# Optimization experiments

Hardware: AMD Instinct MI355X
Metric: run time of the kernel (lower is better)

The kernel has to match this reference:

```python
import jax, jax.numpy as jnp
import numpy as np
import math

DIM, NH, HD = 4096, 32, 128
B, S = 2, 2048
MAX_SEQ, INIT_SLICE = 4096, 2048  # init_slice = max_seq_len - max_prompt_size
NEG = -1e9


def setup_inputs() -> dict:
    key = jax.random.key(0)
    ks = jax.random.split(key, 6)
    x = jax.random.normal(ks[0], (B, S, DIM), dtype=jnp.float32)
    scale = 1.0 / math.sqrt(DIM)
    wq = jax.random.normal(ks[1], (DIM, DIM), dtype=jnp.float32) * scale
    wk = jax.random.normal(ks[2], (DIM, DIM), dtype=jnp.float32) * scale
    wv = jax.random.normal(ks[3], (DIM, DIM), dtype=jnp.float32) * scale
    wo = jax.random.normal(ks[4], (DIM, DIM), dtype=jnp.float32) * scale
    # RoPE frequencies, viewed as real pairs [S, HD//2, 2] = (cos, sin)
    inv_freq = 1.0 / (10000.0 ** (jnp.arange(0, HD, 2, dtype=jnp.float32) / HD))
    ang = jnp.arange(S, dtype=jnp.float32)[:, None] * inv_freq[None, :]  # [S, HD//2]
    freqs_cis_real = jnp.stack([jnp.cos(ang), jnp.sin(ang)], axis=-1)
    # causal additive mask [1,1,S,S]
    mask = jnp.where(jnp.triu(jnp.ones((S, S), dtype=bool), k=1), NEG, 0.0)[None, None].astype(jnp.float32)
    cache_k = jnp.zeros((B, MAX_SEQ, NH, HD), dtype=jnp.float32)
    cache_v = jnp.zeros((B, MAX_SEQ, NH, HD), dtype=jnp.float32)
    return {"x": x, "freqs_cis_real": freqs_cis_real, "mask": mask,
            "wq": wq, "wk": wk, "wv": wv, "wo": wo,
            "cache_k": cache_k, "cache_v": cache_v, "slice_size": 2048}


def _apply_rotary(xq, xk, freqs_cis_real):
    # xq, xk: [b, s, h, d]; pairs along last dim are (real, imag)
    b, s, h, d = xq.shape
    fr = freqs_cis_real[None, :, None, :, 0]  # [1, s, 1, d//2]
    fi = freqs_cis_real[None, :, None, :, 1]

    def rot(t):
        t = t.reshape(b, s, h, d // 2, 2)
        tr, ti = t[..., 0], t[..., 1]
        out = jnp.stack([tr * fr - ti * fi, tr * fi + ti * fr], axis=-1)
        return out.reshape(b, s, h, d)

    return rot(xq), rot(xk)


def reference(x, freqs_cis_real, mask, wq, wk, wv, wo, cache_k, cache_v, slice_size):
    bsz, seqlen, _ = x.shape
    xq = (x @ wq.T).reshape(bsz, seqlen, NH, HD)
    xk = (x @ wk.T).reshape(bsz, seqlen, NH, HD)
    xv = (x @ wv.T).reshape(bsz, seqlen, NH, HD)
    xq, xk = _apply_rotary(xq, xk, freqs_cis_real)
    # prompt-phase (seqlen > 1) cache update: cat(cache[:, :init_slice], new)
    cache_k_new = jnp.concatenate([cache_k[:bsz, :INIT_SLICE], xk], axis=1)
    cache_v_new = jnp.concatenate([cache_v[:bsz, :INIT_SLICE], xv], axis=1)
    keys = cache_k_new[:, -slice_size:]    # [b, k, h, d]
    values = cache_v_new[:, -slice_size:]
    scores = jnp.einsum('bqhd,bkhd->bhqk', xq, keys) / math.sqrt(HD)
    scores = scores + mask
    probs = jax.nn.softmax(scores.astype(jnp.float32), axis=-1).astype(xq.dtype)
    out = jnp.einsum('bhqk,bkhd->bqhd', probs, values).reshape(bsz, seqlen, -1)
    return out @ wo.T
```

## Files before the change

### kernel.cpp

```cpp
#include <hip/hip_runtime.h>
#include <hip/hip_bf16.h>
#include <stdint.h>

#define SEQ   2048
#define NHEAD 32
#define HDIM  128
#define DMODEL 4096
#define MTOT  4096
#define RSCALE 0.08838834764831845f

typedef __hip_bfloat16 bf16_t;
typedef __attribute__((ext_vector_type(8))) short short8v;
typedef __attribute__((ext_vector_type(4))) short short4v;
typedef __attribute__((ext_vector_type(4))) float f32x4;

typedef __attribute__((address_space(3))) void lds_void;
typedef __attribute__((address_space(1))) void gbl_void;
#define TO_LDS(p) ((lds_void*)(uint32_t)(uintptr_t)(p))
#define TO_GBL(p) ((gbl_void*)(uintptr_t)(p))
#define ASYNC_CP16(g, l) __builtin_amdgcn_global_load_lds(TO_GBL(g), TO_LDS(l), 16, 0, 0)

__device__ __forceinline__ float bf2f(short u) {
  union { uint32_t i; float f; } x; x.i = ((uint32_t)(uint16_t)u) << 16; return x.f;
}

__global__ __launch_bounds__(256) void cast4_f32_to_bf16(const float* __restrict__ s0,
                                                         const float* __restrict__ s1,
                                                         const float* __restrict__ s2,
                                                         const float* __restrict__ s3,
                                                         bf16_t* __restrict__ out) {
  const int w = blockIdx.y;
  const float* in = (w == 0) ? s0 : ((w == 1) ? s1 : ((w == 2) ? s2 : s3));
  bf16_t* o = out + (size_t)w * 16777216u;
  size_t i = (size_t)blockIdx.x * 256 + threadIdx.x;
  const f32x4* p = (const f32x4*)in + i * 2;
  f32x4 a = p[0], b = p[1];
  __align__(16) bf16_t tmp[8];
#pragma unroll
  for (int j = 0; j < 4; ++j) tmp[j]     = __float2bfloat16(a[j]);
#pragma unroll
  for (int j = 0; j < 4; ++j) tmp[4 + j] = __float2bfloat16(b[j]);
  *(short8v*)(o + i * 8) = *(const short8v*)tmp;
}

__global__ __launch_bounds__(256) void cast_f32_to_bf16(const float* __restrict__ in,
                                                        bf16_t* __restrict__ out) {
  size_t i = (size_t)blockIdx.x * 256 + threadIdx.x;
  const f32x4* p = (const f32x4*)in + i * 2;
  f32x4 a = p[0], b = p[1];
  __align__(16) bf16_t tmp[8];
#pragma unroll
  for (int j = 0; j < 4; ++j) tmp[j]     = __float2bfloat16(a[j]);
#pragma unroll
  for (int j = 0; j < 4; ++j) tmp[4 + j] = __float2bfloat16(b[j]);
  *(short8v*)(out + i * 8) = *(const short8v*)tmp;
}

#define VMW_(N) asm volatile("s_waitcnt vmcnt(" #N ")" ::: "memory")
#define VMW(N) VMW_(N)
#define SB0 __builtin_amdgcn_sched_barrier(0)

#define STAGE_A(mh_, X)                                                        \
  { const int tr_ = tid >> 3, c_ = tid & 7;                                    \
    _Pragma("unroll")                                                          \
    for (int i_ = 0; i_ < 2; ++i_) {                                           \
      const int row_ = (mh_) * 64 + i_ * 128 + tr_;                            \
      const int cg_ = c_ ^ (row_ & 7);                                         \
      ASYNC_CP16(gA0 + (size_t)row_ * 4096 + (size_t)(X) * 64 + cg_ * 8,       \
                 ldsc + (((X) & 1) << 16) + row_ * 128 + c_ * 16); } }

#define STAGE_B(nh_, X)                                                        \
  { const int tr_ = tid >> 3, c_ = tid & 7;                                    \
    _Pragma("unroll")                                                          \
    for (int i_ = 0; i_ < 2; ++i_) {                                           \
      const int row_ = i_ * 128 + (tr_ >> 5) * 64 + (nh_) * 32 + (tr_ & 31);   \
      const int cg_ = c_ ^ (row_ & 7);                                         \
      ASYNC_CP16(gB0 + (size_t)row_ * 4096 + (size_t)(X) * 64 + cg_ * 8,       \
                 ldsc + (((X) & 1) << 16) + 32768 + row_ * 128 + c_ * 16); } }

#define TILE4(T, DOSTG, VA, VB, VC)                                            \
  {                                                                            \
    const int sb = ((T) & 1) << 16;                                            \
    const int Xn = (T) + 1;                                                    \
    short8v a0[4][2], a1[4][2], b0[2][2], b1[2][2];                            \
                                                 \
    VMW(VA);                                                                   \
    __builtin_amdgcn_s_barrier();                                              \
    SB0;                                                                       \
    if (DOSTG) STAGE_A(0, Xn);                                                 \
    SB0;                                                                       \
    _Pragma("unroll") for (int m = 0; m < 4; ++m)                              \
      _Pragma("unroll") for (int kk = 0; kk < 2; ++kk)                         \
        a0[m][kk] = *(const short8v*)(ldsc + sb + aRow + m * 2048 + (kk ? cx1 : cx0)); \
    _Pragma("unroll") for (int n = 0; n < 2; ++n)                              \
      _Pragma("unroll") for (int kk = 0; kk < 2; ++kk)                         \
        b0[n][kk] = *(const short8v*)(ldsc + sb + bRow + n * 2048 + (kk ? cx1 : cx0)); \
    __builtin_amdgcn_s_setprio(1);                                             \
    _Pragma("unroll") for (int m = 0; m < 4; ++m)                              \
      _Pragma("unroll") for (int n = 0; n < 2; ++n)                            \
        _Pragma("unroll") for (int kk = 0; kk < 2; ++kk)                       \
          acc[m][n] = __builtin_amdgcn_mfma_f32_16x16x32_bf16(a0[m][kk], b0[n][kk], acc[m][n], 0, 0, 0); \
    __builtin_amdgcn_s_setprio(0);                                             \
                                                 \
    VMW(VB);                                                                   \
    __builtin_amdgcn_s_barrier();                                              \
    SB0;                                                                       \
    if (DOSTG) STAGE_B(0, Xn);                                                 \
    SB0;                                                                       \
    _Pragma("unroll") for (int n = 0; n < 2; ++n)                              \
      _Pragma("unroll") for (int kk = 0; kk < 2; ++kk)                         \
        b1[n][kk] = *(const short8v*)(ldsc + sb + bRow + 4096 + n * 2048 + (kk ? cx1 : cx0)); \
    __builtin_amdgcn_s_setprio(1);                                             \
    _Pragma("unroll") for (int m = 0; m < 4; ++m)                              \
      _Pragma("unroll") for (int n = 0; n < 2; ++n)                            \
        _Pragma("unroll") for (int kk = 0; kk < 2; ++kk)                       \
          acc[m][2 + n] = __builtin_amdgcn_mfma_f32_16x16x32_bf16(a0[m][kk], b1[n][kk], acc[m][2 + n], 0, 0, 0); \
    __builtin_amdgcn_s_setprio(0);                                             \
                                                 \
    VMW(VC);                                                                   \
    __builtin_amdgcn_s_barrier();                                              \
    SB0;                                                                       \
    if (DOSTG) STAGE_B(1, Xn);                                                 \
    SB0;                                                                       \
    _Pragma("unroll") for (int m = 0; m < 4; ++m)                              \
      _Pragma("unroll") for (int kk = 0; kk < 2; ++kk)                         \
        a1[m][kk] = *(const short8v*)(ldsc + sb + aRow + 8192 + m * 2048 + (kk ? cx1 : cx0)); \
    __builtin_amdgcn_s_setprio(1);                                             \
    _Pragma("unroll") for (int m = 0; m < 4; ++m)                              \
      _Pragma("unroll") for (int n = 0; n < 2; ++n)                            \
        _Pragma("unroll") for (int kk = 0; kk < 2; ++kk)                       \
          acc[4 + m][2 + n] = __builtin_amdgcn_mfma_f32_16x16x32_bf16(a1[m][kk], b1[n][kk], acc[4 + m][2 + n], 0, 0, 0); \
    __builtin_amdgcn_s_setprio(0);                                             \
                                     \
    if (DOSTG) STAGE_A(1, Xn);                                                 \
    __builtin_amdgcn_s_setprio(1);                                             \
    _Pragma("unroll") for (int m = 0; m < 4; ++m)                              \
      _Pragma("unroll") for (int n = 0; n < 2; ++n)                            \
        _Pragma("unroll") for (int kk = 0; kk < 2; ++kk)                       \
          acc[4 + m][n] = __builtin_amdgcn_mfma_f32_16x16x32_bf16(a1[m][kk], b0[n][kk], acc[4 + m][n], 0, 0, 0); \
    __builtin_amdgcn_s_setprio(0);                                             \
  }

template <bool OUT_BF16>
__global__ __launch_bounds__(512, 2) void gemm_nt(const bf16_t* __restrict__ A,
                                                  const bf16_t* __restrict__ B0,
                                                  const bf16_t* __restrict__ B1,
                                                  const bf16_t* __restrict__ B2,
                                                  void* __restrict__ Cout) {
  __shared__ __align__(16) char ldsbuf[131072];
  char* ldsc = ldsbuf;
  const int z = blockIdx.z;
  const bf16_t* __restrict__ Bm = (z == 0) ? B0 : (z == 1 ? B1 : B2);
  const int tid = threadIdx.x;
  const int wave = tid >> 6, lane = tid & 63;
  const int bid = blockIdx.x;
  const int xcd = bid & 7, idx = bid >> 3;
  const int bm = (xcd >> 1) * 4 + (idx >> 3);
  const int bn = (xcd & 1) * 8 + (idx & 7);
  const int wr = wave >> 2, wc = wave & 3;
  const int r = lane & 15, g = lane >> 4;

  f32x4 acc[8][4] = {};

  const bf16_t* gA0 = A  + (size_t)bm * 256 * 4096;
  const bf16_t* gB0 = Bm + (size_t)bn * 256 * 4096;

  const int swz = r & 7;
  const int cx0 = (g ^ swz) << 4;
  const int cx1 = ((4 + g) ^ swz) << 4;
  const int aRow = (wr * 128 + r) * 128;
  const int bRow = 32768 + (wc * 64 + r) * 128;

  STAGE_A(0, 0);
  STAGE_B(0, 0);
  STAGE_B(1, 0);
  STAGE_A(1, 0);

  for (int T = 0; T < 63; ++T) TILE4(T, 1, 4, 4, 4);
  TILE4(63, 0, 4, 2, 0);

  const size_t row_base = (size_t)bm * 256 + wr * 128 + g * 4;
  const size_t col_base = (size_t)bn * 256 + wc * 64 + r;
  if (OUT_BF16) {
    bf16_t* C = (bf16_t*)Cout + (size_t)z * 16777216u;
#pragma unroll
    for (int m = 0; m < 8; ++m)
#pragma unroll
      for (int n = 0; n < 4; ++n)
#pragma unroll
        for (int j = 0; j < 4; ++j)
          C[(row_base + m * 16 + j) * 4096 + col_base + n * 16] = __float2bfloat16(acc[m][n][j]);
  } else {
    float* C = (float*)Cout;
#pragma unroll
    for (int m = 0; m < 8; ++m)
#pragma unroll
      for (int n = 0; n < 4; ++n)
#pragma unroll
        for (int j = 0; j < 4; ++j)
          C[(row_base + m * 16 + j) * 4096 + col_base + n * 16] = acc[m][n][j];
  }
}

__global__ __launch_bounds__(256) void rope_kernel(const bf16_t* __restrict__ qkv,
                                                   const float* __restrict__ freqs,
                                                   bf16_t* __restrict__ qrot,
                                                   bf16_t* __restrict__ krot) {
  const int which = blockIdx.y;
  const bf16_t* __restrict__ src = qkv + (size_t)which * 16777216u;
  bf16_t* __restrict__ dst = (which == 0) ? qrot : krot;
  const float sc = (which == 0) ? RSCALE : 1.0f;
  size_t t = (size_t)blockIdx.x * 256 + threadIdx.x;
  int dg = t & 15;
  int s  = (int)(t >> 4) & 2047;
  int bh = (int)(t >> 15);
  int b  = bh >> 5;
  int d0 = dg * 8;

  short8v v = *(const short8v*)&src[((size_t)(b * 2048 + s)) * 4096 + (bh & 31) * 128 + d0];
  const float* fp = freqs + (size_t)s * 128 + d0;
  f32x4 f0 = *(const f32x4*)fp;
  f32x4 f1 = *(const f32x4*)(fp + 4);
  float fr[4] = {f0[0], f0[2], f1[0], f1[2]};
  float fi[4] = {f0[1], f0[3], f1[1], f1[3]};
  __align__(16) bf16_t tmp[8];
#pragma unroll
  for (int i = 0; i < 4; ++i) {
    float tr = bf2f(v[2 * i]), ti = bf2f(v[2 * i + 1]);
    tmp[2 * i]     = __float2bfloat16((tr * fr[i] - ti * fi[i]) * sc);
    tmp[2 * i + 1] = __float2bfloat16((tr * fi[i] + ti * fr[i]) * sc);
  }
  *(short8v*)&dst[((size_t)bh * 2048 + s) * 128 + d0] = *(const short8v*)tmp;
}

__global__ __launch_bounds__(256) void vtrans_kernel(const bf16_t* __restrict__ xv,
                                                     bf16_t* __restrict__ vt) {
  __shared__ bf16_t tile[64 * 136];
  const int s0 = blockIdx.x * 64;
  const int bh = blockIdx.y;
  const int b = bh >> 5, h = bh & 31;
  const int tid = threadIdx.x;
#pragma unroll
  for (int it = 0; it < 4; ++it) {
    int c = it * 256 + tid;
    int row = c >> 4, col8 = c & 15;
    short8v v = *(const short8v*)&xv[((size_t)(b * 2048 + s0 + row)) * 4096 + h * 128 + col8 * 8];
    *(short8v*)&tile[row * 136 + col8 * 8] = v;
  }
  __syncthreads();
#pragma unroll
  for (int it = 0; it < 4; ++it) {
    int c = it * 256 + tid;
    int d = c >> 3, sc = c & 7;
    __align__(16) bf16_t tmp[8];
#pragma unroll
    for (int i = 0; i < 8; ++i) tmp[i] = tile[(sc * 8 + i) * 136 + d];
    *(short8v*)&vt[((size_t)(bh * 128 + d)) * 2048 + s0 + sc * 8] = *(const short8v*)tmp;
  }
}

#define PSTR 72
__global__ __launch_bounds__(512) void attn_kernel(const bf16_t* __restrict__ qrot,
                                                   const bf16_t* __restrict__ krot,
                                                   const bf16_t* __restrict__ vt,
                                                   bf16_t* __restrict__ att) {
  __shared__ bf16_t Kls[3][64 * 128];
  __shared__ bf16_t Vls[3][128 * 64];
  __shared__ bf16_t Pls[8][16 * PSTR];

  const int lid  = blockIdx.x;
  const int xcd  = lid & 7;
  const int kk_  = lid >> 3;
  const int bh   = xcd + 8 * ((kk_ >> 4) & 7);
  const int qidx = 15 - (kk_ & 15);
  const int warp = threadIdx.x >> 6;
  const int lane = threadIdx.x & 63;
  const int r = lane & 15, g = lane >> 4;

  const bf16_t* __restrict__ Q  = qrot + (size_t)bh * 2048 * 128;
  const bf16_t* __restrict__ Kp = krot + (size_t)bh * 2048 * 128;
  const bf16_t* __restrict__ Vt = vt   + (size_t)bh * 128 * 2048;
  bf16_t* __restrict__ Pw = &Pls[warp][0];

  const int qB = qidx * 128 + warp * 16;
  const int ntiles = 2 * qidx + 2;

  short8v qf[4];
#pragma unroll
  for (int kk = 0; kk < 4; ++kk)
    qf[kk] = *(const short8v*)&Q[(size_t)(qB + r) * 128 + kk * 32 + g * 8];

  float l = 0.f;
  f32x4 o[8];
#pragma unroll
  for (int n2 = 0; n2 < 8; ++n2) o[n2] = f32x4{0.f, 0.f, 0.f, 0.f};

  const int rA = lane >> 4, cA = lane & 15;
  const int rB = lane >> 3, cB = lane & 7;
  const int swz = (r & 7) << 4;

  auto STG = [&](int kb_, int buf) {
#pragma unroll
    for (int i = 0; i < 2; ++i) {
      const int krow = warp * 8 + i * 4 + rA;
      const int kcol = 8 * (cA ^ (krow & 7));
      ASYNC_CP16(Kp + (size_t)(kb_ + krow) * 128 + kcol,
                 (char*)&Kls[buf][0] + (size_t)(krow * 128 + cA * 8) * 2);
    }
#pragma unroll
    for (int i = 0; i < 2; ++i) {
      const int vrow = warp * 16 + i * 8 + rB;
      const int vcol = 8 * (cB ^ rB);
      ASYNC_CP16(Vt + (size_t)vrow * 2048 + kb_ + vcol,
                 (char*)&Vls[buf][0] + (size_t)(vrow * 64 + cB * 8) * 2);
    }
  };

  STG(0, 0);
  int cur = 0;
  for (int t = 0; t < ntiles; ++t) {
    const int kb = t * 64;
    const int nxt = (cur == 2) ? 0 : cur + 1;
    if (t + 1 < ntiles) {
      STG(kb + 64, nxt);
      VMW(4);
    } else {
      VMW(0);
    }
    __builtin_amdgcn_s_barrier();
    SB0;

    if (kb <= qB + 15) {
      const char* Kc = (const char*)&Kls[cur][0];
      const char* Vc = (const char*)&Vls[cur][0];
      f32x4 sacc[4];
#pragma unroll
      for (int n = 0; n < 4; ++n) sacc[n] = f32x4{0.f, 0.f, 0.f, 0.f};
#pragma unroll
      for (int n = 0; n < 4; ++n)
#pragma unroll
        for (int kk = 0; kk < 4; ++kk) {
          short8v kf = *(const short8v*)(Kc + (n * 16 + r) * 256 + ((kk * 64 + g * 16) ^ swz));
          sacc[n] = __builtin_amdgcn_mfma_f32_16x16x32_bf16(kf, qf[kk], sacc[n], 0, 0, 0);
        }

      float p[16];
#pragma unroll
      for (int n = 0; n < 4; ++n)
#pragma unroll
        for (int j = 0; j < 4; ++j)
          p[n * 4 + j] = __expf(sacc[n][j]);

      if (kb + 63 > qB) {
        const int qa = qB + r;
#pragma unroll
        for (int n = 0; n < 4; ++n)
#pragma unroll
          for (int j = 0; j < 4; ++j)
            if (kb + n * 16 + g * 4 + j > qa) p[n * 4 + j] = 0.f;
      }

      {
        float ts[8];
#pragma unroll
        for (int i = 0; i < 8; ++i) ts[i] = p[i] + p[i + 8];
#pragma unroll
        for (int i = 0; i < 4; ++i) ts[i] += ts[i + 4];
        float rs = (ts[0] + ts[1]) + (ts[2] + ts[3]);
        rs += __shfl_xor(rs, 16, 64);
        rs += __shfl_xor(rs, 32, 64);
        l += rs;
      }

#pragma unroll
      for (int n = 0; n < 4; ++n) {
        __align__(8) bf16_t tp[4];
#pragma unroll
        for (int j = 0; j < 4; ++j) tp[j] = __float2bfloat16(p[n * 4 + j]);
        *(short4v*)&Pw[r * PSTR + n * 16 + g * 4] = *(const short4v*)tp;
      }

#pragma unroll
      for (int kk2 = 0; kk2 < 2; ++kk2) {
        short8v pf = *(const short8v*)&Pw[r * PSTR + kk2 * 32 + g * 8];
#pragma unroll
        for (int n2 = 0; n2 < 8; ++n2) {
          short8v vf = *(const short8v*)(Vc + (n2 * 16 + r) * 128 + ((kk2 * 64 + g * 16) ^ swz));
          o[n2] = __builtin_amdgcn_mfma_f32_16x16x32_bf16(pf, vf, o[n2], 0, 0, 0);
        }
      }
    }
    cur = nxt;
  }

  float lq[4];
#pragma unroll
  for (int j = 0; j < 4; ++j) lq[j] = 1.0f / __shfl(l, g * 4 + j, 64);
  const int b = bh >> 5, h = bh & 31;
#pragma unroll
  for (int n2 = 0; n2 < 8; ++n2)
#pragma unroll
    for (int j = 0; j < 4; ++j)
      att[((size_t)(b * 2048 + qB + g * 4 + j)) * 4096 + h * 128 + n2 * 16 + r] =
          __float2bfloat16(o[n2][j] * lq[j]);
}

extern "C" void kernel_launch(void* const* d_in, const int* in_sizes, int n_in,
                              void* d_out, int out_size, void* d_ws, size_t ws_size,
                              hipStream_t stream) {
  (void)in_sizes; (void)n_in; (void)out_size; (void)ws_size;
  const float* x  = (const float*)d_in[0];
  const float* fr = (const float*)d_in[1];
  const float* wq = (const float*)d_in[3];
  const float* wk = (const float*)d_in[4];
  const float* wv = (const float*)d_in[5];
  const float* wo = (const float*)d_in[6];

  char* ws = (char*)d_ws;
  const size_t MB32 = 33554432;
  bf16_t* xb  = (bf16_t*)(ws + 0 * MB32);
  bf16_t* wqb = (bf16_t*)(ws + 1 * MB32);
  bf16_t* wkb = (bf16_t*)(ws + 2 * MB32);
  bf16_t* wvb = (bf16_t*)(ws + 3 * MB32);
  bf16_t* qkv = (bf16_t*)(ws + 4 * MB32);

  cast4_f32_to_bf16<<<dim3(8192, 4), 256, 0, stream>>>(x, wq, wk, wv, xb);

  gemm_nt<true><<<dim3(256, 1, 3), 512, 0, stream>>>(xb, wqb, wkb, wvb, (void*)qkv);

  bf16_t* qrot = xb;
  bf16_t* krot = wqb;
  bf16_t* vtp  = wkb;
  bf16_t* attb = wvb;

  rope_kernel<<<dim3(8192, 2), 256, 0, stream>>>(qkv, fr, qrot, krot);
  vtrans_kernel<<<dim3(32, 64), 256, 0, stream>>>(qkv + 2 * 16777216u, vtp);

  bf16_t* wob = qkv;
  cast_f32_to_bf16<<<8192, 256, 0, stream>>>(wo, wob);

  attn_kernel<<<1024, 512, 0, stream>>>(qrot, krot, vtp, attb);

  gemm_nt<false><<<dim3(256, 1, 1), 512, 0, stream>>>(attb, wob, wob, wob, d_out);
}
```

Measured before the change: 676.9 us.

## Fuse RoPE and V transpose into QKV GEMM epilogue, reorder LDS staging

The QKV GEMM epilogue now applies rotary embedding (with the query scale) using a lane shuffle to fetch each pair partner, and writes V directly in transposed layout. This removes the separate rope and vtrans kernels and their round trip of the QKV intermediate through global memory. Inside the GEMM tile loop, async global-to-LDS staging is moved after the LDS fragment reads and followed by an explicit lgkmcnt wait. The block-to-tile mapping across XCDs is also changed. In exchange, the epilogue does scattered 2-byte and 8-byte stores and extra freq loads per element, which may slow the GEMM tail.

```diff
diff --git a/kernel.cpp b/kernel.cpp
--- a/kernel.cpp
+++ b/kernel.cpp
@@ -87,14 +87,15 @@
     VMW(VA);                                                                   \
     __builtin_amdgcn_s_barrier();                                              \
     SB0;                                                                       \
-    if (DOSTG) STAGE_A(0, Xn);                                                 \
-    SB0;                                                                       \
     _Pragma("unroll") for (int m = 0; m < 4; ++m)                              \
       _Pragma("unroll") for (int kk = 0; kk < 2; ++kk)                         \
         a0[m][kk] = *(const short8v*)(ldsc + sb + aRow + m * 2048 + (kk ? cx1 : cx0)); \
     _Pragma("unroll") for (int n = 0; n < 2; ++n)                              \
       _Pragma("unroll") for (int kk = 0; kk < 2; ++kk)                         \
         b0[n][kk] = *(const short8v*)(ldsc + sb + bRow + n * 2048 + (kk ? cx1 : cx0)); \
+    if (DOSTG) STAGE_A(0, Xn);                                                 \
+    asm volatile("s_waitcnt lgkmcnt(0)" ::: "memory");                         \
+    SB0;                                                                       \
     __builtin_amdgcn_s_setprio(1);                                             \
     _Pragma("unroll") for (int m = 0; m < 4; ++m)                              \
       _Pragma("unroll") for (int n = 0; n < 2; ++n)                            \
@@ -105,11 +106,12 @@
     VMW(VB);                                                                   \
     __builtin_amdgcn_s_barrier();                                              \
     SB0;                                                                       \
-    if (DOSTG) STAGE_B(0, Xn);                                                 \
-    SB0;                                                                       \
     _Pragma("unroll") for (int n = 0; n < 2; ++n)                              \
       _Pragma("unroll") for (int kk = 0; kk < 2; ++kk)                         \
         b1[n][kk] = *(const short8v*)(ldsc + sb + bRow + 4096 + n * 2048 + (kk ? cx1 : cx0)); \
+    if (DOSTG) STAGE_B(0, Xn);                                                 \
+    asm volatile("s_waitcnt lgkmcnt(0)" ::: "memory");                         \
+    SB0;                                                                       \
     __builtin_amdgcn_s_setprio(1);                                             \
     _Pragma("unroll") for (int m = 0; m < 4; ++m)                              \
       _Pragma("unroll") for (int n = 0; n < 2; ++n)                            \
@@ -120,11 +122,12 @@
     VMW(VC);                                                                   \
     __builtin_amdgcn_s_barrier();                                              \
     SB0;                                                                       \
-    if (DOSTG) STAGE_B(1, Xn);                                                 \
-    SB0;                                                                       \
     _Pragma("unroll") for (int m = 0; m < 4; ++m)                              \
       _Pragma("unroll") for (int kk = 0; kk < 2; ++kk)                         \
         a1[m][kk] = *(const short8v*)(ldsc + sb + aRow + 8192 + m * 2048 + (kk ? cx1 : cx0)); \
+    if (DOSTG) STAGE_B(1, Xn);                                                 \
+    asm volatile("s_waitcnt lgkmcnt(0)" ::: "memory");                         \
+    SB0;                                                                       \
     __builtin_amdgcn_s_setprio(1);                                             \
     _Pragma("unroll") for (int m = 0; m < 4; ++m)                              \
       _Pragma("unroll") for (int n = 0; n < 2; ++n)                            \
@@ -141,12 +144,15 @@
     __builtin_amdgcn_s_setprio(0);                                             \
   }
 
-template <bool OUT_BF16>
+template <int MODE>
 __global__ __launch_bounds__(512, 2) void gemm_nt(const bf16_t* __restrict__ A,
                                                   const bf16_t* __restrict__ B0,
                                                   const bf16_t* __restrict__ B1,
                                                   const bf16_t* __restrict__ B2,
-                                                  void* __restrict__ Cout) {
+                                                  void* __restrict__ out0,
+                                                  bf16_t* __restrict__ out1,
+                                                  bf16_t* __restrict__ out2,
+                                                  const float* __restrict__ freqs) {
   __shared__ __align__(16) char ldsbuf[131072];
   char* ldsc = ldsbuf;
   const int z = blockIdx.z;
@@ -155,8 +161,8 @@
   const int wave = tid >> 6, lane = tid & 63;
   const int bid = blockIdx.x;
   const int xcd = bid & 7, idx = bid >> 3;
-  const int bm = (xcd >> 1) * 4 + (idx >> 3);
-  const int bn = (xcd & 1) * 8 + (idx & 7);
+  const int bm = xcd * 2 + (idx >> 4);
+  const int bn = idx & 15;
   const int wr = wave >> 2, wc = wave & 3;
   const int r = lane & 15, g = lane >> 4;
 
@@ -179,83 +185,57 @@
   for (int T = 0; T < 63; ++T) TILE4(T, 1, 4, 4, 4);
   TILE4(63, 0, 4, 2, 0);
 
-  const size_t row_base = (size_t)bm * 256 + wr * 128 + g * 4;
-  const size_t col_base = (size_t)bn * 256 + wc * 64 + r;
-  if (OUT_BF16) {
-    bf16_t* C = (bf16_t*)Cout + (size_t)z * 16777216u;
+  const int row0 = bm * 256 + wr * 128 + g * 4;
+  const int col0 = bn * 256 + wc * 64;
+
+  if (MODE == 0) {
+    float* C = (float*)out0;
 #pragma unroll
     for (int m = 0; m < 8; ++m)
 #pragma unroll
       for (int n = 0; n < 4; ++n)
 #pragma unroll
         for (int j = 0; j < 4; ++j)
-          C[(row_base + m * 16 + j) * 4096 + col_base + n * 16] = __float2bfloat16(acc[m][n][j]);
+          C[(size_t)(row0 + m * 16 + j) * 4096 + col0 + n * 16 + r] = acc[m][n][j];
+  } else if (z == 2) {
+    bf16_t* VT = out2;
+#pragma unroll
+    for (int m = 0; m < 8; ++m) {
+      const int row = row0 + m * 16;
+      const int b = row >> 11, s = row & 2047;
+#pragma unroll
+      for (int n = 0; n < 4; ++n) {
+        const int col = col0 + n * 16 + r;
+        const int h = col >> 7, d = col & 127;
+        __align__(8) bf16_t tp[4];
+#pragma unroll
+        for (int j = 0; j < 4; ++j) tp[j] = __float2bfloat16(acc[m][n][j]);
+        *(short4v*)&VT[((size_t)(b * 32 + h) * 128 + d) * 2048 + s] = *(const short4v*)tp;
+      }
+    }
   } else {
-    float* C = (float*)Cout;
+    bf16_t* dst = (z == 0) ? (bf16_t*)out0 : out1;
+    const float scl = (z == 0) ? RSCALE : 1.0f;
+    const float sgn = (r & 1) ? 1.0f : -1.0f;
 #pragma unroll
     for (int m = 0; m < 8; ++m)
 #pragma unroll
-      for (int n = 0; n < 4; ++n)
-#pragma unroll
-        for (int j = 0; j < 4; ++j)
-          C[(row_base + m * 16 + j) * 4096 + col_base + n * 16] = acc[m][n][j];
-  }
-}
-
-__global__ __launch_bounds__(256) void rope_kernel(const bf16_t* __restrict__ qkv,
-                                                   const float* __restrict__ freqs,
-                                                   bf16_t* __restrict__ qrot,
-                                                   bf16_t* __restrict__ krot) {
-  const int which = blockIdx.y;
-  const bf16_t* __restrict__ src = qkv + (size_t)which * 16777216u;
-  bf16_t* __restrict__ dst = (which == 0) ? qrot : krot;
-  const float sc = (which == 0) ? RSCALE : 1.0f;
-  size_t t = (size_t)blockIdx.x * 256 + threadIdx.x;
-  int dg = t & 15;
-  int s  = (int)(t >> 4) & 2047;
-  int bh = (int)(t >> 15);
-  int b  = bh >> 5;
-  int d0 = dg * 8;
-
-  short8v v = *(const short8v*)&src[((size_t)(b * 2048 + s)) * 4096 + (bh & 31) * 128 + d0];
-  const float* fp = freqs + (size_t)s * 128 + d0;
-  f32x4 f0 = *(const f32x4*)fp;
-  f32x4 f1 = *(const f32x4*)(fp + 4);
-  float fr[4] = {f0[0], f0[2], f1[0], f1[2]};
-  float fi[4] = {f0[1], f0[3], f1[1], f1[3]};
-  __align__(16) bf16_t tmp[8];
-#pragma unroll
-  for (int i = 0; i < 4; ++i) {
-    float tr = bf2f(v[2 * i]), ti = bf2f(v[2 * i + 1]);
-    tmp[2 * i]     = __float2bfloat16((tr * fr[i] - ti * fi[i]) * sc);
-    tmp[2 * i + 1] = __float2bfloat16((tr * fi[i] + ti * fr[i]) * sc);
-  }
-  *(short8v*)&dst[((size_t)bh * 2048 + s) * 128 + d0] = *(const short8v*)tmp;
-}
-
-__global__ __launch_bounds__(256) void vtrans_kernel(const bf16_t* __restrict__ xv,
-                                                     bf16_t* __restrict__ vt) {
-  __shared__ bf16_t tile[64 * 136];
-  const int s0 = blockIdx.x * 64;
-  const int bh = blockIdx.y;
-  const int b = bh >> 5, h = bh & 31;
-  const int tid = threadIdx.x;
-#pragma unroll
-  for (int it = 0; it < 4; ++it) {
-    int c = it * 256 + tid;
-    int row = c >> 4, col8 = c & 15;
-    short8v v = *(const short8v*)&xv[((size_t)(b * 2048 + s0 + row)) * 4096 + h * 128 + col8 * 8];
-    *(short8v*)&tile[row * 136 + col8 * 8] = v;
-  }
-  __syncthreads();
-#pragma unroll
-  for (int it = 0; it < 4; ++it) {
-    int c = it * 256 + tid;
-    int d = c >> 3, sc = c & 7;
-    __align__(16) bf16_t tmp[8];
-#pragma unroll
-    for (int i = 0; i < 8; ++i) tmp[i] = tile[(sc * 8 + i) * 136 + d];
-    *(short8v*)&vt[((size_t)(bh * 128 + d)) * 2048 + s0 + sc * 8] = *(const short8v*)tmp;
+      for (int j = 0; j < 4; ++j) {
+        const int row = row0 + m * 16 + j;
+        const int b = row >> 11, s = row & 2047;
+#pragma unroll
+        for (int n = 0; n < 4; ++n) {
+          const int col = col0 + n * 16 + r;
+          const int h = col >> 7, d = col & 127;
+          const float self = acc[m][n][j];
+          const float part = __shfl_xor(self, 1, 64);
+          const float* fp = freqs + (size_t)s * 128 + (d >> 1) * 2;
+          const float frv = fp[0] * scl;
+          const float fiv = fp[1] * scl * sgn;
+          dst[((size_t)(b * 32 + h) * 2048 + s) * 128 + d] =
+              __float2bfloat16(self * frv + part * fiv);
+        }
+      }
   }
 }
 
@@ -418,28 +398,25 @@
 
   char* ws = (char*)d_ws;
   const size_t MB32 = 33554432;
-  bf16_t* xb  = (bf16_t*)(ws + 0 * MB32);
-  bf16_t* wqb = (bf16_t*)(ws + 1 * MB32);
-  bf16_t* wkb = (bf16_t*)(ws + 2 * MB32);
-  bf16_t* wvb = (bf16_t*)(ws + 3 * MB32);
-  bf16_t* qkv = (bf16_t*)(ws + 4 * MB32);
+  bf16_t* xb   = (bf16_t*)(ws + 0 * MB32);
+  bf16_t* wqb  = (bf16_t*)(ws + 1 * MB32);
+  bf16_t* wkb  = (bf16_t*)(ws + 2 * MB32);
+  bf16_t* wvb  = (bf16_t*)(ws + 3 * MB32);
+  bf16_t* qrot = (bf16_t*)(ws + 4 * MB32);
+  bf16_t* krot = (bf16_t*)(ws + 5 * MB32);
+  bf16_t* vtp  = (bf16_t*)(ws + 6 * MB32);
 
   cast4_f32_to_bf16<<<dim3(8192, 4), 256, 0, stream>>>(x, wq, wk, wv, xb);
 
-  gemm_nt<true><<<dim3(256, 1, 3), 512, 0, stream>>>(xb, wqb, wkb, wvb, (void*)qkv);
-
-  bf16_t* qrot = xb;
-  bf16_t* krot = wqb;
-  bf16_t* vtp  = wkb;
-  bf16_t* attb = wvb;
-
-  rope_kernel<<<dim3(8192, 2), 256, 0, stream>>>(qkv, fr, qrot, krot);
-  vtrans_kernel<<<dim3(32, 64), 256, 0, stream>>>(qkv + 2 * 16777216u, vtp);
-
-  bf16_t* wob = qkv;
+  gemm_nt<1><<<dim3(256, 1, 3), 512, 0, stream>>>(xb, wqb, wkb, wvb,
+                                                  (void*)qrot, krot, vtp, fr);
+
+  bf16_t* wob  = wqb;
+  bf16_t* attb = xb;
   cast_f32_to_bf16<<<8192, 256, 0, stream>>>(wo, wob);
 
   attn_kernel<<<1024, 512, 0, stream>>>(qrot, krot, vtp, attb);
 
-  gemm_nt<false><<<dim3(256, 1, 1), 512, 0, stream>>>(attb, wob, wob, wob, d_out);
-}
+  gemm_nt<0><<<dim3(256, 1, 1), 512, 0, stream>>>(attb, wob, wob, wob,
+                                                  d_out, nullptr, nullptr, nullptr);
+}
```

After: 654.9 us. -3.3%, faster.
